# Performance work log

Hardware: AMD Instinct MI355X
Metric: run time of the kernel (lower is better)

Reference implementation:

```python
import jax, jax.numpy as jnp
import numpy as np

H = 512     # LSTM_HIDDEN_SIZE
IN = 64     # LSTM_INPUT_SIZE
B = 256
T = 512
OUT = 96    # output_size (decode horizon)


def setup_inputs() -> dict:
    key = jax.random.key(0)
    ks = jax.random.split(key, 32)
    k = 1.0 / np.sqrt(H)
    u = lambda kk, shape: jax.random.uniform(kk, shape, jnp.float32, -k, k)
    inp = {"inputs": jax.random.normal(ks[0], (B, T, IN), jnp.float32)}
    shapes = {
        "enc_Wih0": (4 * H, IN), "enc_Whh0": (4 * H, H), "enc_bih0": (4 * H,), "enc_bhh0": (4 * H,),
        "enc_Wih1": (4 * H, H),  "enc_Whh1": (4 * H, H), "enc_bih1": (4 * H,), "enc_bhh1": (4 * H,),
        "dec_Wih0": (4 * H, 1),  "dec_Whh0": (4 * H, H), "dec_bih0": (4 * H,), "dec_bhh0": (4 * H,),
        "dec_Wih1": (4 * H, H),  "dec_Whh1": (4 * H, H), "dec_bih1": (4 * H,), "dec_bhh1": (4 * H,),
        "proj_W": (1, H), "proj_b": (1,),
    }
    for i, (name, sh) in enumerate(shapes.items()):
        inp[name] = u(ks[i + 1], sh)
    inp["output_size"] = OUT
    return inp


def lstm_cell(x, h, c, Wih, Whh, bih, bhh):
    # PyTorch gate order: i, f, g, o
    z = x @ Wih.T + h @ Whh.T + (bih + bhh)
    i, f, g, o = jnp.split(z, 4, axis=-1)
    c_new = jax.nn.sigmoid(f) * c + jax.nn.sigmoid(i) * jnp.tanh(g)
    h_new = jax.nn.sigmoid(o) * jnp.tanh(c_new)
    return h_new, c_new


def reference(inputs,
              enc_Wih0, enc_Whh0, enc_bih0, enc_bhh0,
              enc_Wih1, enc_Whh1, enc_bih1, enc_bhh1,
              dec_Wih0, dec_Whh0, dec_bih0, dec_bhh0,
              dec_Wih1, dec_Whh1, dec_bih1, dec_bhh1,
              proj_W, proj_b, output_size):
    bsz = inputs.shape[0]
    hdim = enc_Whh0.shape[1]
    z = jnp.zeros((bsz, hdim), inputs.dtype)

    # ---- encoder: 2-layer LSTM over time (batch_first -> time-major scan) ----
    def enc_step(carry, x_t):
        h0, c0, h1, c1 = carry
        h0, c0 = lstm_cell(x_t, h0, c0, enc_Wih0, enc_Whh0, enc_bih0, enc_bhh0)
        h1, c1 = lstm_cell(h0, h1, c1, enc_Wih1, enc_Whh1, enc_bih1, enc_bhh1)
        return (h0, c0, h1, c1), None

    xs = jnp.swapaxes(inputs, 0, 1)  # [T, B, IN]
    (h0, c0, h1, c1), _ = jax.lax.scan(enc_step, (z, z, z, z), xs)

    def dec_step(carry, _):
        h0, c0, h1, c1, x = carry  # x: [B, 1]
        h0, c0 = lstm_cell(x, h0, c0, dec_Wih0, dec_Whh0, dec_bih0, dec_bhh0)
        h1, c1 = lstm_cell(h0, h1, c1, dec_Wih1, dec_Whh1, dec_bih1, dec_bhh1)
        y = h1 @ proj_W.T + proj_b  # [B, 1]
        return (h0, c0, h1, c1, y), y

    x0 = jnp.zeros((bsz, 1), inputs.dtype)
    _, ys = jax.lax.scan(dec_step, (h0, c0, h1, c1, x0), None, length=output_size)
    # ys: [OUT, B, 1] -> [B, OUT, 1]
    return jnp.swapaxes(ys, 0, 1)
```

## Files before the change

### kernel.cpp

```cpp
#include <hip/hip_runtime.h>
#include <math.h>

#define Bb   256
#define Tt   512
#define INn  64
#define Hh   512
#define OUTn 96
#define NWG  256
#define TPB  512
#define SP   (Hh*Bb)
#define RSTRIDE 36
#define HDR  8192

struct Params {
  const float *Xt;
  float *H0, *H1;
  unsigned int *flags;
  unsigned int *rel;
  const float *Wih0,*Whh0,*bih0,*bhh0,*Wih1,*Whh1,*bih1,*bhh1;
  const float *dWih0,*dWhh0,*dbih0,*dbhh0,*dWih1,*dWhh1,*dbih1,*dbhh1;
  const float *projW,*projb;
  float *out;
};

__device__ __forceinline__ float sigm(float x){ return 1.0f/(1.0f + expf(-x)); }

__device__ __forceinline__ void gridbar(unsigned int* flags, unsigned int* rel,
                                        unsigned int g) {
  __syncthreads();
  const int tid = threadIdx.x;
  if (blockIdx.x == 0) {
    if (tid > 0 && tid < NWG) {
      while (__hip_atomic_load(&flags[tid*16], __ATOMIC_RELAXED, __HIP_MEMORY_SCOPE_AGENT) < g)
        __builtin_amdgcn_s_sleep(1);
    }
    __syncthreads();
    if (tid == 0) {
      __threadfence();
      __hip_atomic_store(rel, g, __ATOMIC_RELEASE, __HIP_MEMORY_SCOPE_AGENT);
    }
    __syncthreads();
  } else {
    if (tid == 0) {
      __threadfence();
      __hip_atomic_store(&flags[blockIdx.x*16], g, __ATOMIC_RELEASE, __HIP_MEMORY_SCOPE_AGENT);
      while (__hip_atomic_load(rel, __ATOMIC_RELAXED, __HIP_MEMORY_SCOPE_AGENT) < g)
        __builtin_amdgcn_s_sleep(1);
      __threadfence();
    }
    __syncthreads();
  }
}

__global__ void __launch_bounds__(256) xpose(const float* __restrict__ X, float* __restrict__ Xt) {
  __shared__ float tile[64][65];
  const int t = blockIdx.x;
  const int l = threadIdx.x & 63;
  const int r = threadIdx.x >> 6;
  for (int qd = 0; qd < 4; ++qd) {
    #pragma unroll
    for (int rep = 0; rep < 16; ++rep) {
      int bl = rep*4 + r;
      tile[bl][l] = X[(size_t)(qd*64 + bl)*(Tt*INn) + (size_t)t*INn + l];
    }
    __syncthreads();
    #pragma unroll
    for (int rep = 0; rep < 16; ++rep) {
      int i = rep*4 + r;
      Xt[(size_t)t*(INn*Bb) + (size_t)i*Bb + qd*64 + l] = tile[l][i];
    }
    __syncthreads();
  }
}

__global__ void __launch_bounds__(TPB, 2) lstm_main(Params P) {
  __shared__ float WA[512][32];
  __shared__ float WB[512][16];
  __shared__ float WX[64][16];
  __shared__ float BS[32];
  __shared__ float PW[Hh];
  __shared__ float WXD[16];
  __shared__ float PBs;
  __shared__ float RED[2][128][RSTRIDE];

  const int tid = threadIdx.x;
  const int w   = blockIdx.x;
  const int uw  = w >> 1;
  const int bh  = w & 1;
  const int bq  = tid & 31;
  const int h   = (tid >> 5) & 3;
  const int kh  = tid >> 7;
  const int j   = 4*uw + h;
  const int h8  = h*8, h4 = h*4;
  const int slot = h*32 + bq;
  const int boff = 128*bh + 4*bq;
  unsigned int bgen = 1;

  for (int e = tid; e < 512*32; e += TPB) {
    int k = e >> 5, c = e & 31, hh = c >> 3, s = c & 7;
    int unit = 4*uw + hh;
    WA[k][c] = (s < 4) ? P.Wih1[(size_t)(s*Hh + unit)*Hh + k]
                       : P.Whh0[(size_t)((s-4)*Hh + unit)*Hh + k];
  }
  for (int e = tid; e < 512*16; e += TPB) {
    int k = e >> 4, c = e & 15, hh = c >> 2, g = c & 3;
    WB[k][c] = P.Whh1[(size_t)(g*Hh + 4*uw + hh)*Hh + k];
  }
  for (int e = tid; e < 64*16; e += TPB) {
    int k = e >> 4, c = e & 15, hh = c >> 2, g = c & 3;
    WX[k][c] = P.Wih0[(size_t)(g*Hh + 4*uw + hh)*INn + k];
  }
  if (tid < 32) {
    int c = tid, hh = c >> 3, s = c & 7;
    int unit = 4*uw + hh;
    BS[c] = (s < 4) ? (P.bih1[s*Hh+unit] + P.bhh1[s*Hh+unit])
                    : (P.bih0[(s-4)*Hh+unit] + P.bhh0[(s-4)*Hh+unit]);
  }
  __syncthreads();

  float c0[4] = {0,0,0,0}, c1[4] = {0,0,0,0};

  float4 eA_h[4], eA_g[4], eB_h[4], eB_g[4];

#define ENC_LOAD(HB, GB, K0)                                              \
  _Pragma("unroll")                                                       \
  for (int t = 0; t < 4; ++t) {                                           \
    HB[t] = *reinterpret_cast<const float4*>(&h0in[((K0)+t)*Bb]);         \
    GB[t] = *reinterpret_cast<const float4*>(&h1in[((K0)+t)*Bb]);         \
  }

#define ENC_COMPUTE(HB, GB, K0)                                           \
  _Pragma("unroll")                                                       \
  for (int t = 0; t < 4; ++t) {                                           \
    const int k = (K0) + t;                                               \
    const float4 w1 = *reinterpret_cast<const float4*>(&WA[k][h8]);       \
    const float4 w0 = *reinterpret_cast<const float4*>(&WA[k][h8+4]);     \
    const float4 wb = *reinterpret_cast<const float4*>(&WB[k][h4]);       \
    const float* hv = &HB[t].x;                                           \
    const float* gv = &GB[t].x;                                           \
    _Pragma("unroll")                                                     \
    for (int m = 0; m < 4; ++m) {                                         \
      z1i[m]=fmaf(w1.x,hv[m],z1i[m]); z1f[m]=fmaf(w1.y,hv[m],z1f[m]);     \
      z1g[m]=fmaf(w1.z,hv[m],z1g[m]); z1o[m]=fmaf(w1.w,hv[m],z1o[m]);     \
      z0i[m]=fmaf(w0.x,hv[m],z0i[m]); z0f[m]=fmaf(w0.y,hv[m],z0f[m]);     \
      z0g[m]=fmaf(w0.z,hv[m],z0g[m]); z0o[m]=fmaf(w0.w,hv[m],z0o[m]);     \
      z1i[m]=fmaf(wb.x,gv[m],z1i[m]); z1f[m]=fmaf(wb.y,gv[m],z1f[m]);     \
      z1g[m]=fmaf(wb.z,gv[m],z1g[m]); z1o[m]=fmaf(wb.w,gv[m],z1o[m]);     \
    }                                                                     \
  }

  for (int p = -1; p <= 511; ++p) {
    float z1i[4], z1f[4], z1g[4], z1o[4];
    float z0i[4], z0f[4], z0g[4], z0o[4];
    #pragma unroll
    for (int m = 0; m < 4; ++m) {
      z1i[m] = (kh==0) ? BS[h8+0] : 0.f; z1f[m] = (kh==0) ? BS[h8+1] : 0.f;
      z1g[m] = (kh==0) ? BS[h8+2] : 0.f; z1o[m] = (kh==0) ? BS[h8+3] : 0.f;
      z0i[m] = (kh==0) ? BS[h8+4] : 0.f; z0f[m] = (kh==0) ? BS[h8+5] : 0.f;
      z0g[m] = (kh==0) ? BS[h8+6] : 0.f; z0o[m] = (kh==0) ? BS[h8+7] : 0.f;
    }
    const float* __restrict__ h0in = P.H0 + (size_t)(p & 1)*SP + boff;
    const float* __restrict__ h1in = P.H1 + (size_t)((p+1) & 1)*SP + boff;
    const int kb = kh*128, ke = kb + 128;

    ENC_LOAD(eA_h, eA_g, kb);

    {
      int tx = (p+1 < Tt) ? (p+1) : (Tt-1);
      const float* __restrict__ xin = P.Xt + (size_t)tx*(INn*Bb) + boff;
      #pragma unroll 4
      for (int k = kh*16; k < kh*16 + 16; ++k) {
        const float4 wv = *reinterpret_cast<const float4*>(&WX[k][h4]);
        const float4 xv4 = *reinterpret_cast<const float4*>(&xin[k*Bb]);
        const float* xv = &xv4.x;
        #pragma unroll
        for (int m = 0; m < 4; ++m) {
          z0i[m]=fmaf(wv.x,xv[m],z0i[m]); z0f[m]=fmaf(wv.y,xv[m],z0f[m]);
          z0g[m]=fmaf(wv.z,xv[m],z0g[m]); z0o[m]=fmaf(wv.w,xv[m],z0o[m]);
        }
      }
    }
    for (int kk = kb; kk < ke; kk += 8) {
      ENC_LOAD(eB_h, eB_g, kk+4);
      ENC_COMPUTE(eA_h, eA_g, kk);
      const int kn = (kk+8 < ke) ? (kk+8) : kb;
      ENC_LOAD(eA_h, eA_g, kn);
      ENC_COMPUTE(eB_h, eB_g, kk+4);
    }

    if (kh >= 2) {
      float* r = &RED[kh-2][slot][0];
      *reinterpret_cast<float4*>(&r[ 0]) = make_float4(z1i[0],z1i[1],z1i[2],z1i[3]);
      *reinterpret_cast<float4*>(&r[ 4]) = make_float4(z1f[0],z1f[1],z1f[2],z1f[3]);
      *reinterpret_cast<float4*>(&r[ 8]) = make_float4(z1g[0],z1g[1],z1g[2],z1g[3]);
      *reinterpret_cast<float4*>(&r[12]) = make_float4(z1o[0],z1o[1],z1o[2],z1o[3]);
      *reinterpret_cast<float4*>(&r[16]) = make_float4(z0i[0],z0i[1],z0i[2],z0i[3]);
      *reinterpret_cast<float4*>(&r[20]) = make_float4(z0f[0],z0f[1],z0f[2],z0f[3]);
      *reinterpret_cast<float4*>(&r[24]) = make_float4(z0g[0],z0g[1],z0g[2],z0g[3]);
      *reinterpret_cast<float4*>(&r[28]) = make_float4(z0o[0],z0o[1],z0o[2],z0o[3]);
    }
    __syncthreads();
    if (kh < 2) {
      float* r = &RED[kh][slot][0];
      {
        const float* rr = r;
        #pragma unroll
        for (int m = 0; m < 4; ++m) {
          z1i[m]+=rr[ 0+m]; z1f[m]+=rr[ 4+m]; z1g[m]+=rr[ 8+m]; z1o[m]+=rr[12+m];
          z0i[m]+=rr[16+m]; z0f[m]+=rr[20+m]; z0g[m]+=rr[24+m]; z0o[m]+=rr[28+m];
        }
      }
      if (kh == 1) {
        *reinterpret_cast<float4*>(&r[ 0]) = make_float4(z1i[0],z1i[1],z1i[2],z1i[3]);
        *reinterpret_cast<float4*>(&r[ 4]) = make_float4(z1f[0],z1f[1],z1f[2],z1f[3]);
        *reinterpret_cast<float4*>(&r[ 8]) = make_float4(z1g[0],z1g[1],z1g[2],z1g[3]);
        *reinterpret_cast<float4*>(&r[12]) = make_float4(z1o[0],z1o[1],z1o[2],z1o[3]);
        *reinterpret_cast<float4*>(&r[16]) = make_float4(z0i[0],z0i[1],z0i[2],z0i[3]);
        *reinterpret_cast<float4*>(&r[20]) = make_float4(z0f[0],z0f[1],z0f[2],z0f[3]);
        *reinterpret_cast<float4*>(&r[24]) = make_float4(z0g[0],z0g[1],z0g[2],z0g[3]);
        *reinterpret_cast<float4*>(&r[28]) = make_float4(z0o[0],z0o[1],z0o[2],z0o[3]);
      }
    }
    __syncthreads();
    if (kh == 0) {
      const float* rr = &RED[1][slot][0];
      #pragma unroll
      for (int m = 0; m < 4; ++m) {
        z1i[m]+=rr[ 0+m]; z1f[m]+=rr[ 4+m]; z1g[m]+=rr[ 8+m]; z1o[m]+=rr[12+m];
        z0i[m]+=rr[16+m]; z0f[m]+=rr[20+m]; z0g[m]+=rr[24+m]; z0o[m]+=rr[28+m];
      }
      if (p >= 0) {
        float* st = P.H1 + (size_t)(p & 1)*SP + (size_t)j*Bb + boff;
        float4 o; float* ov = &o.x;
        #pragma unroll
        for (int m = 0; m < 4; ++m) {
          c1[m] = sigm(z1f[m])*c1[m] + sigm(z1i[m])*tanhf(z1g[m]);
          ov[m] = sigm(z1o[m])*tanhf(c1[m]);
        }
        *reinterpret_cast<float4*>(st) = o;
      }
      if (p < 511) {
        float* st = P.H0 + (size_t)((p+1) & 1)*SP + (size_t)j*Bb + boff;
        float4 o; float* ov = &o.x;
        #pragma unroll
        for (int m = 0; m < 4; ++m) {
          c0[m] = sigm(z0f[m])*c0[m] + sigm(z0i[m])*tanhf(z0g[m]);
          ov[m] = sigm(z0o[m])*tanhf(c0[m]);
        }
        *reinterpret_cast<float4*>(st) = o;
      }
    }
    gridbar(P.flags, P.rel, bgen); ++bgen;
  }

  for (int e = tid; e < 512*32; e += TPB) {
    int k = e >> 5, c = e & 31, hh = c >> 3, s = c & 7;
    int unit = 4*uw + hh;
    WA[k][c] = (s < 4) ? P.dWih1[(size_t)(s*Hh + unit)*Hh + k]
                       : P.dWhh1[(size_t)((s-4)*Hh + unit)*Hh + k];
  }
  for (int e = tid; e < 512*16; e += TPB) {
    int k = e >> 4, c = e & 15, hh = c >> 2, g = c & 3;
    WB[k][c] = P.dWhh0[(size_t)(g*Hh + 4*uw + hh)*Hh + k];
  }
  if (tid < 16) {
    int c = tid, hh = c >> 2, g = c & 3;
    WXD[c] = P.dWih0[g*Hh + 4*uw + hh];
  }
  if (tid >= 32 && tid < 64) {
    int c = tid - 32, hh = c >> 3, s = c & 7;
    int unit = 4*uw + hh;
    BS[c] = (s < 4) ? (P.dbih1[s*Hh+unit] + P.dbhh1[s*Hh+unit])
                    : (P.dbih0[(s-4)*Hh+unit] + P.dbhh0[(s-4)*Hh+unit]);
  }
  for (int k = tid; k < Hh; k += TPB) PW[k] = P.projW[k];
  if (tid == 0) PBs = P.projb[0];
  __syncthreads();

  for (int q = 0; q < OUTn; ++q) {
    float xq[4];
    #pragma unroll
    for (int m = 0; m < 4; ++m) xq[m] = (kh==0 && q>0) ? PBs : 0.f;
    if (q > 0) {
      const float* __restrict__ h1p = P.H1 + (size_t)((q+1)&1)*SP + boff;
      const int kb = kh*128, ke = kb + 128;
      #pragma unroll 4
      for (int k = kb; k < ke; ++k) {
        float pw = PW[k];
        const float4 hp4 = *reinterpret_cast<const float4*>(&h1p[k*Bb]);
        const float* hp = &hp4.x;
        #pragma unroll
        for (int m = 0; m < 4; ++m) xq[m] = fmaf(pw, hp[m], xq[m]);
      }
    }
    float zd[4][4];
    #pragma unroll
    for (int g = 0; g < 4; ++g)
      #pragma unroll
      for (int m = 0; m < 4; ++m)
        zd[g][m] = (kh==0) ? BS[h8+4+g] : 0.f;
    {
      const float* __restrict__ h0p = P.H0 + (size_t)((q+1)&1)*SP + boff;
      const int kb = kh*128, ke = kb + 128;
      #pragma unroll 4
      for (int k = kb; k < ke; ++k) {
        const float4 wv = *reinterpret_cast<const float4*>(&WB[k][h4]);
        const float4 hv4 = *reinterpret_cast<const float4*>(&h0p[k*Bb]);
        const float* hv = &hv4.x;
        #pragma unroll
        for (int m = 0; m < 4; ++m) {
          zd[0][m]=fmaf(wv.x,hv[m],zd[0][m]); zd[1][m]=fmaf(wv.y,hv[m],zd[1][m]);
          zd[2][m]=fmaf(wv.z,hv[m],zd[2][m]); zd[3][m]=fmaf(wv.w,hv[m],zd[3][m]);
        }
      }
    }
    if (kh >= 2) {
      float* r = &RED[kh-2][slot][0];
      #pragma unroll
      for (int g = 0; g < 4; ++g)
        *reinterpret_cast<float4*>(&r[g*4]) = make_float4(zd[g][0],zd[g][1],zd[g][2],zd[g][3]);
      *reinterpret_cast<float4*>(&r[16]) = make_float4(xq[0],xq[1],xq[2],xq[3]);
    }
    __syncthreads();
    if (kh < 2) {
      float* r = &RED[kh][slot][0];
      #pragma unroll
      for (int g = 0; g < 4; ++g) {
        const float4 v = *reinterpret_cast<const float4*>(&r[g*4]);
        zd[g][0]+=v.x; zd[g][1]+=v.y; zd[g][2]+=v.z; zd[g][3]+=v.w;
      }
      {
        const float4 v = *reinterpret_cast<const float4*>(&r[16]);
        xq[0]+=v.x; xq[1]+=v.y; xq[2]+=v.z; xq[3]+=v.w;
      }
      if (kh == 1) {
        #pragma unroll
        for (int g = 0; g < 4; ++g)
          *reinterpret_cast<float4*>(&r[g*4]) = make_float4(zd[g][0],zd[g][1],zd[g][2],zd[g][3]);
        *reinterpret_cast<float4*>(&r[16]) = make_float4(xq[0],xq[1],xq[2],xq[3]);
      }
    }
    __syncthreads();
    if (kh == 0) {
      const float* r = &RED[1][slot][0];
      #pragma unroll
      for (int g = 0; g < 4; ++g) {
        const float4 v = *reinterpret_cast<const float4*>(&r[g*4]);
        zd[g][0]+=v.x; zd[g][1]+=v.y; zd[g][2]+=v.z; zd[g][3]+=v.w;
      }
      {
        const float4 v = *reinterpret_cast<const float4*>(&r[16]);
        xq[0]+=v.x; xq[1]+=v.y; xq[2]+=v.z; xq[3]+=v.w;
      }
      if (uw == 0 && h == 0 && q > 0) {
        #pragma unroll
        for (int m = 0; m < 4; ++m) P.out[(size_t)(boff + m)*OUTn + (q-1)] = xq[m];
      }
      float* st = P.H0 + (size_t)(q&1)*SP + (size_t)j*Bb + boff;
      float4 o; float* ov = &o.x;
      #pragma unroll
      for (int m = 0; m < 4; ++m) {
        float zi = fmaf(WXD[h4+0], xq[m], zd[0][m]);
        float zf = fmaf(WXD[h4+1], xq[m], zd[1][m]);
        float zg = fmaf(WXD[h4+2], xq[m], zd[2][m]);
        float zo = fmaf(WXD[h4+3], xq[m], zd[3][m]);
        c0[m] = sigm(zf)*c0[m] + sigm(zi)*tanhf(zg);
        ov[m] = sigm(zo)*tanhf(c0[m]);
      }
      *reinterpret_cast<float4*>(st) = o;
    }
    gridbar(P.flags, P.rel, bgen); ++bgen;

    float y[4][4];
    #pragma unroll
    for (int g = 0; g < 4; ++g)
      #pragma unroll
      for (int m = 0; m < 4; ++m)
        y[g][m] = (kh==0) ? BS[h8+g] : 0.f;
    {
      const float* __restrict__ h0c = P.H0 + (size_t)(q&1)*SP + boff;
      const float* __restrict__ h1q = P.H1 + (size_t)((q+1)&1)*SP + boff;
      const int kb = kh*128, ke = kb + 128;
      #pragma unroll 4
      for (int k = kb; k < ke; ++k) {
        const float4 w1 = *reinterpret_cast<const float4*>(&WA[k][h8]);
        const float4 w2 = *reinterpret_cast<const float4*>(&WA[k][h8+4]);
        const float4 av4 = *reinterpret_cast<const float4*>(&h0c[k*Bb]);
        const float4 dv4 = *reinterpret_cast<const float4*>(&h1q[k*Bb]);
        const float* av = &av4.x;
        const float* dv = &dv4.x;
        #pragma unroll
        for (int m = 0; m < 4; ++m) {
          y[0][m]=fmaf(w1.x,av[m],y[0][m]); y[1][m]=fmaf(w1.y,av[m],y[1][m]);
          y[2][m]=fmaf(w1.z,av[m],y[2][m]); y[3][m]=fmaf(w1.w,av[m],y[3][m]);
          y[0][m]=fmaf(w2.x,dv[m],y[0][m]); y[1][m]=fmaf(w2.y,dv[m],y[1][m]);
          y[2][m]=fmaf(w2.z,dv[m],y[2][m]); y[3][m]=fmaf(w2.w,dv[m],y[3][m]);
        }
      }
    }
    if (kh >= 2) {
      float* r = &RED[kh-2][slot][0];
      #pragma unroll
      for (int g = 0; g < 4; ++g)
        *reinterpret_cast<float4*>(&r[g*4]) = make_float4(y[g][0],y[g][1],y[g][2],y[g][3]);
    }
    __syncthreads();
    if (kh < 2) {
      float* r = &RED[kh][slot][0];
      #pragma unroll
      for (int g = 0; g < 4; ++g) {
        const float4 v = *reinterpret_cast<const float4*>(&r[g*4]);
        y[g][0]+=v.x; y[g][1]+=v.y; y[g][2]+=v.z; y[g][3]+=v.w;
      }
      if (kh == 1) {
        #pragma unroll
        for (int g = 0; g < 4; ++g)
          *reinterpret_cast<float4*>(&r[g*4]) = make_float4(y[g][0],y[g][1],y[g][2],y[g][3]);
      }
    }
    __syncthreads();
    if (kh == 0) {
      const float* r = &RED[1][slot][0];
      #pragma unroll
      for (int g = 0; g < 4; ++g) {
        const float4 v = *reinterpret_cast<const float4*>(&r[g*4]);
        y[g][0]+=v.x; y[g][1]+=v.y; y[g][2]+=v.z; y[g][3]+=v.w;
      }
      float* st = P.H1 + (size_t)(q&1)*SP + (size_t)j*Bb + boff;
      float4 o; float* ov = &o.x;
      #pragma unroll
      for (int m = 0; m < 4; ++m) {
        c1[m] = sigm(y[1][m])*c1[m] + sigm(y[0][m])*tanhf(y[2][m]);
        ov[m] = sigm(y[3][m])*tanhf(c1[m]);
      }
      *reinterpret_cast<float4*>(st) = o;
    }
    gridbar(P.flags, P.rel, bgen); ++bgen;
  }

  if (kh == 0 && uw == 0 && h == 0) {
    const float* __restrict__ h1f = P.H1 + (size_t)((OUTn-1)&1)*SP + boff;
    float acc[4] = {PBs, PBs, PBs, PBs};
    #pragma unroll 4
    for (int k = 0; k < Hh; ++k) {
      float pw = PW[k];
      const float4 hp4 = *reinterpret_cast<const float4*>(&h1f[k*Bb]);
      const float* hp = &hp4.x;
      #pragma unroll
      for (int m = 0; m < 4; ++m) acc[m] = fmaf(pw, hp[m], acc[m]);
    }
    #pragma unroll
    for (int m = 0; m < 4; ++m) P.out[(size_t)(boff + m)*OUTn + (OUTn-1)] = acc[m];
  }
}

extern "C" void kernel_launch(void* const* d_in, const int* in_sizes, int n_in,
                              void* d_out, int out_size, void* d_ws, size_t ws_size,
                              hipStream_t stream) {
  Params P;
  const float* X = (const float*)d_in[0];
  P.Wih0  = (const float*)d_in[1];  P.Whh0  = (const float*)d_in[2];
  P.bih0  = (const float*)d_in[3];  P.bhh0  = (const float*)d_in[4];
  P.Wih1  = (const float*)d_in[5];  P.Whh1  = (const float*)d_in[6];
  P.bih1  = (const float*)d_in[7];  P.bhh1  = (const float*)d_in[8];
  P.dWih0 = (const float*)d_in[9];  P.dWhh0 = (const float*)d_in[10];
  P.dbih0 = (const float*)d_in[11]; P.dbhh0 = (const float*)d_in[12];
  P.dWih1 = (const float*)d_in[13]; P.dWhh1 = (const float*)d_in[14];
  P.dbih1 = (const float*)d_in[15]; P.dbhh1 = (const float*)d_in[16];
  P.projW = (const float*)d_in[17]; P.projb = (const float*)d_in[18];

  float* ws = (float*)d_ws;
  P.flags = (unsigned int*)ws;
  P.rel   = (unsigned int*)ws + 4096;
  P.H0  = ws + HDR;
  P.H1  = ws + HDR + 2*SP;
  float* Xt = ws + HDR + 4*SP;
  P.Xt  = Xt;
  P.out = (float*)d_out;

  hipMemsetAsync(d_ws, 0, (size_t)(HDR + 4*SP)*sizeof(float), stream);
  hipLaunchKernelGGL(xpose, dim3(Tt), dim3(256), 0, stream, X, Xt);

  void* args[] = { &P };
  hipLaunchCooperativeKernel((void*)lstm_main, dim3(NWG), dim3(TPB), args, 0, stream);
}
```

Before: 26.97 ms.

## Split LSTM work across 512 cooperative workgroups with wave-shuffle K reduction

Adds a new persistent kernel that launches 512 workgroups, each owning 2 hidden units instead of 4, which halves the per-block weight slice held in LDS. The K dimension is now split across lanes within a wave and reduced with xor shuffles, replacing the LDS-based cross-wave reduction and its extra __syncthreads. The grid barrier is parameterised by workgroup count, and the old kernel stays as a fallback when occupancy does not allow 512 co-resident blocks. The cost is a barrier with twice as many participants and some redundant activation math across lanes.

```diff
diff --git a/kernel.cpp b/kernel.cpp
--- a/kernel.cpp
+++ b/kernel.cpp
@@ -6,11 +6,10 @@
 #define INn  64
 #define Hh   512
 #define OUTn 96
-#define NWG  256
 #define TPB  512
 #define SP   (Hh*Bb)
 #define RSTRIDE 36
-#define HDR  8192
+#define HDR  12288
 
 struct Params {
   const float *Xt;
@@ -26,11 +25,11 @@
 __device__ __forceinline__ float sigm(float x){ return 1.0f/(1.0f + expf(-x)); }
 
 __device__ __forceinline__ void gridbar(unsigned int* flags, unsigned int* rel,
-                                        unsigned int g) {
+                                        unsigned int g, int nwg) {
   __syncthreads();
   const int tid = threadIdx.x;
   if (blockIdx.x == 0) {
-    if (tid > 0 && tid < NWG) {
+    if (tid > 0 && tid < nwg) {
       while (__hip_atomic_load(&flags[tid*16], __ATOMIC_RELAXED, __HIP_MEMORY_SCOPE_AGENT) < g)
         __builtin_amdgcn_s_sleep(1);
     }
@@ -73,7 +72,282 @@
   }
 }
 
-__global__ void __launch_bounds__(TPB, 2) lstm_main(Params P) {
+#define BFLY4(a)                                                   \
+  do { _Pragma("unroll")                                           \
+    for (int m_ = 0; m_ < 4; ++m_) {                               \
+      a[m_] += __shfl_xor(a[m_], 8, 64);                           \
+      a[m_] += __shfl_xor(a[m_], 16, 64);                          \
+      a[m_] += __shfl_xor(a[m_], 32, 64);                          \
+    } } while (0)
+
+__global__ void __launch_bounds__(TPB, 2) lstm512(Params P) {
+  __shared__ float WA[512][20];
+  __shared__ float WB[512][8];
+  __shared__ float WX[64][8];
+  __shared__ float BS[16];
+  __shared__ float PW[Hh];
+  __shared__ float WXD[8];
+  __shared__ float PBs;
+
+  const int tid  = threadIdx.x;
+  const int lane = tid & 63;
+  const int kh   = lane >> 3;
+  const int bqlo = lane & 7;
+  const int bqhi = (tid >> 6) & 3;
+  const int h    = tid >> 8;
+  const int bq   = bqhi*8 + bqlo;
+  const int uw   = blockIdx.x >> 1;
+  const int bh   = blockIdx.x & 1;
+  const int j    = 2*uw + h;
+  const int h8   = h*8, h4 = h*4;
+  const int boff = 128*bh + 4*bq;
+  unsigned int bgen = 1;
+
+  for (int e = tid; e < 512*16; e += TPB) {
+    int k = e >> 4, c = e & 15, hh = c >> 3, s = c & 7;
+    int unit = 2*uw + hh;
+    WA[k][c] = (s < 4) ? P.Wih1[(size_t)(s*Hh + unit)*Hh + k]
+                       : P.Whh0[(size_t)((s-4)*Hh + unit)*Hh + k];
+  }
+  for (int e = tid; e < 512*8; e += TPB) {
+    int k = e >> 3, c = e & 7, hh = c >> 2, g = c & 3;
+    WB[k][c] = P.Whh1[(size_t)(g*Hh + 2*uw + hh)*Hh + k];
+  }
+  for (int e = tid; e < 64*8; e += TPB) {
+    int k = e >> 3, c = e & 7, hh = c >> 2, g = c & 3;
+    WX[k][c] = P.Wih0[(size_t)(g*Hh + 2*uw + hh)*INn + k];
+  }
+  if (tid < 16) {
+    int c = tid, hh = c >> 3, s = c & 7;
+    int unit = 2*uw + hh;
+    BS[c] = (s < 4) ? (P.bih1[s*Hh+unit] + P.bhh1[s*Hh+unit])
+                    : (P.bih0[(s-4)*Hh+unit] + P.bhh0[(s-4)*Hh+unit]);
+  }
+  __syncthreads();
+
+  float c0[4] = {0,0,0,0}, c1[4] = {0,0,0,0};
+
+  for (int p = -1; p <= 511; ++p) {
+    float z1i[4], z1f[4], z1g[4], z1o[4];
+    float z0i[4], z0f[4], z0g[4], z0o[4];
+    #pragma unroll
+    for (int m = 0; m < 4; ++m) {
+      z1i[m] = (kh==0) ? BS[h8+0] : 0.f; z1f[m] = (kh==0) ? BS[h8+1] : 0.f;
+      z1g[m] = (kh==0) ? BS[h8+2] : 0.f; z1o[m] = (kh==0) ? BS[h8+3] : 0.f;
+      z0i[m] = (kh==0) ? BS[h8+4] : 0.f; z0f[m] = (kh==0) ? BS[h8+5] : 0.f;
+      z0g[m] = (kh==0) ? BS[h8+6] : 0.f; z0o[m] = (kh==0) ? BS[h8+7] : 0.f;
+    }
+    const float* __restrict__ h0in = P.H0 + (size_t)(p & 1)*SP + boff;
+    const float* __restrict__ h1in = P.H1 + (size_t)((p+1) & 1)*SP + boff;
+    #pragma unroll 4
+    for (int kk = 0; kk < 64; ++kk) {
+      const int k = kk*8 + kh;
+      const float4 w1 = *reinterpret_cast<const float4*>(&WA[k][h8]);
+      const float4 w0 = *reinterpret_cast<const float4*>(&WA[k][h8+4]);
+      const float4 wb = *reinterpret_cast<const float4*>(&WB[k][h4]);
+      const float4 hv4 = *reinterpret_cast<const float4*>(&h0in[k*Bb]);
+      const float4 gv4 = *reinterpret_cast<const float4*>(&h1in[k*Bb]);
+      const float* hv = &hv4.x;
+      const float* gv = &gv4.x;
+      #pragma unroll
+      for (int m = 0; m < 4; ++m) {
+        z1i[m]=fmaf(w1.x,hv[m],z1i[m]); z1f[m]=fmaf(w1.y,hv[m],z1f[m]);
+        z1g[m]=fmaf(w1.z,hv[m],z1g[m]); z1o[m]=fmaf(w1.w,hv[m],z1o[m]);
+        z0i[m]=fmaf(w0.x,hv[m],z0i[m]); z0f[m]=fmaf(w0.y,hv[m],z0f[m]);
+        z0g[m]=fmaf(w0.z,hv[m],z0g[m]); z0o[m]=fmaf(w0.w,hv[m],z0o[m]);
+        z1i[m]=fmaf(wb.x,gv[m],z1i[m]); z1f[m]=fmaf(wb.y,gv[m],z1f[m]);
+        z1g[m]=fmaf(wb.z,gv[m],z1g[m]); z1o[m]=fmaf(wb.w,gv[m],z1o[m]);
+      }
+    }
+    {
+      int tx = (p+1 < Tt) ? (p+1) : (Tt-1);
+      const float* __restrict__ xin = P.Xt + (size_t)tx*(INn*Bb) + boff;
+      #pragma unroll
+      for (int kk = 0; kk < 8; ++kk) {
+        const int k = kk*8 + kh;
+        const float4 wv = *reinterpret_cast<const float4*>(&WX[k][h4]);
+        const float4 xv4 = *reinterpret_cast<const float4*>(&xin[k*Bb]);
+        const float* xv = &xv4.x;
+        #pragma unroll
+        for (int m = 0; m < 4; ++m) {
+          z0i[m]=fmaf(wv.x,xv[m],z0i[m]); z0f[m]=fmaf(wv.y,xv[m],z0f[m]);
+          z0g[m]=fmaf(wv.z,xv[m],z0g[m]); z0o[m]=fmaf(wv.w,xv[m],z0o[m]);
+        }
+      }
+    }
+    BFLY4(z1i); BFLY4(z1f); BFLY4(z1g); BFLY4(z1o);
+    BFLY4(z0i); BFLY4(z0f); BFLY4(z0g); BFLY4(z0o);
+
+    if (p >= 0) {
+      float4 o; float* ov = &o.x;
+      #pragma unroll
+      for (int m = 0; m < 4; ++m) {
+        c1[m] = sigm(z1f[m])*c1[m] + sigm(z1i[m])*tanhf(z1g[m]);
+        ov[m] = sigm(z1o[m])*tanhf(c1[m]);
+      }
+      if (kh == 0)
+        *reinterpret_cast<float4*>(P.H1 + (size_t)(p & 1)*SP + (size_t)j*Bb + boff) = o;
+    }
+    if (p < 511) {
+      float4 o; float* ov = &o.x;
+      #pragma unroll
+      for (int m = 0; m < 4; ++m) {
+        c0[m] = sigm(z0f[m])*c0[m] + sigm(z0i[m])*tanhf(z0g[m]);
+        ov[m] = sigm(z0o[m])*tanhf(c0[m]);
+      }
+      if (kh == 0)
+        *reinterpret_cast<float4*>(P.H0 + (size_t)((p+1) & 1)*SP + (size_t)j*Bb + boff) = o;
+    }
+    gridbar(P.flags, P.rel, bgen, 512); ++bgen;
+  }
+
+  for (int e = tid; e < 512*16; e += TPB) {
+    int k = e >> 4, c = e & 15, hh = c >> 3, s = c & 7;
+    int unit = 2*uw + hh;
+    WA[k][c] = (s < 4) ? P.dWih1[(size_t)(s*Hh + unit)*Hh + k]
+                       : P.dWhh1[(size_t)((s-4)*Hh + unit)*Hh + k];
+  }
+  for (int e = tid; e < 512*8; e += TPB) {
+    int k = e >> 3, c = e & 7, hh = c >> 2, g = c & 3;
+    WB[k][c] = P.dWhh0[(size_t)(g*Hh + 2*uw + hh)*Hh + k];
+  }
+  if (tid < 8) {
+    int c = tid, hh = c >> 2, g = c & 3;
+    WXD[c] = P.dWih0[g*Hh + 2*uw + hh];
+  }
+  if (tid >= 16 && tid < 32) {
+    int c = tid - 16, hh = c >> 3, s = c & 7;
+    int unit = 2*uw + hh;
+    BS[c] = (s < 4) ? (P.dbih1[s*Hh+unit] + P.dbhh1[s*Hh+unit])
+                    : (P.dbih0[(s-4)*Hh+unit] + P.dbhh0[(s-4)*Hh+unit]);
+  }
+  for (int k = tid; k < Hh; k += TPB) PW[k] = P.projW[k];
+  if (tid == 0) PBs = P.projb[0];
+  __syncthreads();
+
+  for (int q = 0; q < OUTn; ++q) {
+    float xq[4] = {0,0,0,0};
+    if (q > 0) {
+      const float* __restrict__ h1p = P.H1 + (size_t)((q+1)&1)*SP + boff;
+      float acc[4] = {0,0,0,0};
+      #pragma unroll 4
+      for (int kk = 0; kk < 64; ++kk) {
+        const int k = kk*8 + kh;
+        float pw = PW[k];
+        const float4 hp4 = *reinterpret_cast<const float4*>(&h1p[k*Bb]);
+        const float* hp = &hp4.x;
+        #pragma unroll
+        for (int m = 0; m < 4; ++m) acc[m] = fmaf(pw, hp[m], acc[m]);
+      }
+      BFLY4(acc);
+      #pragma unroll
+      for (int m = 0; m < 4; ++m) xq[m] = acc[m] + PBs;
+      if (uw == 0 && h == 0 && kh == 0) {
+        #pragma unroll
+        for (int m = 0; m < 4; ++m) P.out[(size_t)(boff + m)*OUTn + (q-1)] = xq[m];
+      }
+    }
+    float zdi[4], zdf[4], zdg[4], zdo[4];
+    #pragma unroll
+    for (int m = 0; m < 4; ++m) {
+      zdi[m] = (kh==0) ? BS[h8+4] : 0.f; zdf[m] = (kh==0) ? BS[h8+5] : 0.f;
+      zdg[m] = (kh==0) ? BS[h8+6] : 0.f; zdo[m] = (kh==0) ? BS[h8+7] : 0.f;
+    }
+    {
+      const float* __restrict__ h0p = P.H0 + (size_t)((q+1)&1)*SP + boff;
+      #pragma unroll 4
+      for (int kk = 0; kk < 64; ++kk) {
+        const int k = kk*8 + kh;
+        const float4 wv = *reinterpret_cast<const float4*>(&WB[k][h4]);
+        const float4 hv4 = *reinterpret_cast<const float4*>(&h0p[k*Bb]);
+        const float* hv = &hv4.x;
+        #pragma unroll
+        for (int m = 0; m < 4; ++m) {
+          zdi[m]=fmaf(wv.x,hv[m],zdi[m]); zdf[m]=fmaf(wv.y,hv[m],zdf[m]);
+          zdg[m]=fmaf(wv.z,hv[m],zdg[m]); zdo[m]=fmaf(wv.w,hv[m],zdo[m]);
+        }
+      }
+    }
+    BFLY4(zdi); BFLY4(zdf); BFLY4(zdg); BFLY4(zdo);
+    {
+      float4 o; float* ov = &o.x;
+      #pragma unroll
+      for (int m = 0; m < 4; ++m) {
+        float zi = fmaf(WXD[h4+0], xq[m], zdi[m]);
+        float zf = fmaf(WXD[h4+1], xq[m], zdf[m]);
+        float zg = fmaf(WXD[h4+2], xq[m], zdg[m]);
+        float zo = fmaf(WXD[h4+3], xq[m], zdo[m]);
+        c0[m] = sigm(zf)*c0[m] + sigm(zi)*tanhf(zg);
+        ov[m] = sigm(zo)*tanhf(c0[m]);
+      }
+      if (kh == 0)
+        *reinterpret_cast<float4*>(P.H0 + (size_t)(q&1)*SP + (size_t)j*Bb + boff) = o;
+    }
+    gridbar(P.flags, P.rel, bgen, 512); ++bgen;
+
+    float yi[4], yf[4], yg[4], yo[4];
+    #pragma unroll
+    for (int m = 0; m < 4; ++m) {
+      yi[m] = (kh==0) ? BS[h8+0] : 0.f; yf[m] = (kh==0) ? BS[h8+1] : 0.f;
+      yg[m] = (kh==0) ? BS[h8+2] : 0.f; yo[m] = (kh==0) ? BS[h8+3] : 0.f;
+    }
+    {
+      const float* __restrict__ h0c = P.H0 + (size_t)(q&1)*SP + boff;
+      const float* __restrict__ h1q = P.H1 + (size_t)((q+1)&1)*SP + boff;
+      #pragma unroll 4
+      for (int kk = 0; kk < 64; ++kk) {
+        const int k = kk*8 + kh;
+        const float4 w1 = *reinterpret_cast<const float4*>(&WA[k][h8]);
+        const float4 w2 = *reinterpret_cast<const float4*>(&WA[k][h8+4]);
+        const float4 av4 = *reinterpret_cast<const float4*>(&h0c[k*Bb]);
+        const float4 dv4 = *reinterpret_cast<const float4*>(&h1q[k*Bb]);
+        const float* av = &av4.x;
+        const float* dv = &dv4.x;
+        #pragma unroll
+        for (int m = 0; m < 4; ++m) {
+          yi[m]=fmaf(w1.x,av[m],yi[m]); yf[m]=fmaf(w1.y,av[m],yf[m]);
+          yg[m]=fmaf(w1.z,av[m],yg[m]); yo[m]=fmaf(w1.w,av[m],yo[m]);
+          yi[m]=fmaf(w2.x,dv[m],yi[m]); yf[m]=fmaf(w2.y,dv[m],yf[m]);
+          yg[m]=fmaf(w2.z,dv[m],yg[m]); yo[m]=fmaf(w2.w,dv[m],yo[m]);
+        }
+      }
+    }
+    BFLY4(yi); BFLY4(yf); BFLY4(yg); BFLY4(yo);
+    {
+      float4 o; float* ov = &o.x;
+      #pragma unroll
+      for (int m = 0; m < 4; ++m) {
+        c1[m] = sigm(yf[m])*c1[m] + sigm(yi[m])*tanhf(yg[m]);
+        ov[m] = sigm(yo[m])*tanhf(c1[m]);
+      }
+      if (kh == 0)
+        *reinterpret_cast<float4*>(P.H1 + (size_t)(q&1)*SP + (size_t)j*Bb + boff) = o;
+    }
+    gridbar(P.flags, P.rel, bgen, 512); ++bgen;
+  }
+
+  if (uw == 0 && h == 0) {
+    const float* __restrict__ h1f = P.H1 + (size_t)((OUTn-1)&1)*SP + boff;
+    float acc[4] = {0,0,0,0};
+    #pragma unroll 4
+    for (int kk = 0; kk < 64; ++kk) {
+      const int k = kk*8 + kh;
+      float pw = PW[k];
+      const float4 hp4 = *reinterpret_cast<const float4*>(&h1f[k*Bb]);
+      const float* hp = &hp4.x;
+      #pragma unroll
+      for (int m = 0; m < 4; ++m) acc[m] = fmaf(pw, hp[m], acc[m]);
+    }
+    BFLY4(acc);
+    if (kh == 0) {
+      #pragma unroll
+      for (int m = 0; m < 4; ++m)
+        P.out[(size_t)(boff + m)*OUTn + (OUTn-1)] = acc[m] + PBs;
+    }
+  }
+}
+
+__global__ void __launch_bounds__(TPB, 2) lstm_fb(Params P) {
   __shared__ float WA[512][32];
   __shared__ float WB[512][16];
   __shared__ float WX[64][16];
@@ -119,7 +393,6 @@
   __syncthreads();
 
   float c0[4] = {0,0,0,0}, c1[4] = {0,0,0,0};
-
   float4 eA_h[4], eA_g[4], eB_h[4], eB_g[4];
 
 #define ENC_LOAD(HB, GB, K0)                                              \
@@ -128,7 +401,6 @@
     HB[t] = *reinterpret_cast<const float4*>(&h0in[((K0)+t)*Bb]);         \
     GB[t] = *reinterpret_cast<const float4*>(&h1in[((K0)+t)*Bb]);         \
   }
-
 #define ENC_COMPUTE(HB, GB, K0)                                           \
   _Pragma("unroll")                                                       \
   for (int t = 0; t < 4; ++t) {                                           \
@@ -164,7 +436,6 @@
     const int kb = kh*128, ke = kb + 128;
 
     ENC_LOAD(eA_h, eA_g, kb);
-
     {
       int tx = (p+1 < Tt) ? (p+1) : (Tt-1);
       const float* __restrict__ xin = P.Xt + (size_t)tx*(INn*Bb) + boff;
@@ -250,7 +521,7 @@
         *reinterpret_cast<float4*>(st) = o;
       }
     }
-    gridbar(P.flags, P.rel, bgen); ++bgen;
+    gridbar(P.flags, P.rel, bgen, 256); ++bgen;
   }
 
   for (int e = tid; e < 512*32; e += TPB) {
@@ -369,7 +640,7 @@
       }
       *reinterpret_cast<float4*>(st) = o;
     }
-    gridbar(P.flags, P.rel, bgen); ++bgen;
+    gridbar(P.flags, P.rel, bgen, 256); ++bgen;
 
     float y[4][4];
     #pragma unroll
@@ -435,7 +706,7 @@
       }
       *reinterpret_cast<float4*>(st) = o;
     }
-    gridbar(P.flags, P.rel, bgen); ++bgen;
+    gridbar(P.flags, P.rel, bgen, 256); ++bgen;
   }
 
   if (kh == 0 && uw == 0 && h == 0) {
@@ -471,7 +742,7 @@
 
   float* ws = (float*)d_ws;
   P.flags = (unsigned int*)ws;
-  P.rel   = (unsigned int*)ws + 4096;
+  P.rel   = (unsigned int*)ws + 8192;
   P.H0  = ws + HDR;
   P.H1  = ws + HDR + 2*SP;
   float* Xt = ws + HDR + 4*SP;
@@ -482,5 +753,14 @@
   hipLaunchKernelGGL(xpose, dim3(Tt), dim3(256), 0, stream, X, Xt);
 
   void* args[] = { &P };
-  hipLaunchCooperativeKernel((void*)lstm_main, dim3(NWG), dim3(TPB), args, 0, stream);
+  int occ = 0;
+  hipError_t qe = hipOccupancyMaxActiveBlocksPerMultiprocessor(
+      &occ, (const void*)lstm512, TPB, 0);
+  hipError_t le = hipErrorUnknown;
+  if (qe == hipSuccess && occ >= 2)
+    le = hipLaunchCooperativeKernel((void*)lstm512, dim3(512), dim3(TPB), args, 0, stream);
+  if (le != hipSuccess) {
+    (void)hipGetLastError();
+    hipLaunchCooperativeKernel((void*)lstm_fb, dim3(256), dim3(TPB), args, 0, stream);
+  }
 }
```

Result: faster. 25.91 ms (-4.0%).
